# Kernel optimization log

Hardware: AMD Instinct MI355X
Metric: run time of the kernel (lower is better)

## Reference

```python
import jax, jax.numpy as jnp
import numpy as np

L = 2        # n_layers
IN = 172     # in_channels
HID = 128    # hidden_channels
NH = 4       # heads
HD = HID // NH  # per-head dim = 32
TD = 100     # time_dim
V = 400000   # global node table size
N = 150000   # sampled subgraph nodes
E = 500000   # edges per layer
B = 15000    # seed batch size


def setup_inputs() -> dict:
    key = jax.random.key(0)
    ks = jax.random.split(key, 24)
    p = lambda k, shp, s=0.05: jax.random.normal(k, shp, jnp.float32) * s
    inp = {
        "x_all": jax.random.normal(ks[0], (V, IN), jnp.float32),
        "all_node_ids": jax.random.randint(ks[1], (N,), 0, V),
        "edge_src": jax.random.randint(ks[2], (L, E), 0, N),
        "edge_dst": jax.random.randint(ks[3], (L, E), 0, N),
        "dts": jax.random.uniform(ks[4], (L, E), jnp.float32, 0.0, 1e4),
        "batch_size": B,
        # TimeEncode params
        "basis_freq": jnp.asarray(1.0 / 10 ** np.linspace(0, 9, TD), jnp.float32),
        "phase": jnp.zeros((TD,), jnp.float32),
        # input projection
        "Wp": p(ks[5], (IN, HID)), "bp": jnp.zeros((HID,), jnp.float32),
        # per-layer TransformerConv params (stacked over L)
        "Wq": p(ks[6], (L, HID, HID)), "bq": jnp.zeros((L, HID), jnp.float32),
        "Wk": p(ks[7], (L, HID, HID)), "bk": jnp.zeros((L, HID), jnp.float32),
        "Wv": p(ks[8], (L, HID, HID)), "bv": jnp.zeros((L, HID), jnp.float32),
        "We": p(ks[9], (L, TD, HID)),  # lin_edge, bias=False in PyG
        "Wskip": p(ks[10], (L, HID, HID)), "bskip": jnp.zeros((L, HID), jnp.float32),
        "bn_g": jnp.ones((L, HID), jnp.float32), "bn_b": jnp.zeros((L, HID), jnp.float32),
        # classifier head
        "W1": p(ks[11], (HID, HID)), "b1": jnp.zeros((HID,), jnp.float32),
        "g1": jnp.ones((HID,), jnp.float32), "be1": jnp.zeros((HID,), jnp.float32),
        "W2": p(ks[12], (HID, HID // 2)), "b2": jnp.zeros((HID // 2,), jnp.float32),
        "g2": jnp.ones((HID // 2,), jnp.float32), "be2": jnp.zeros((HID // 2,), jnp.float32),
        "W3": p(ks[13], (HID // 2, 1)), "b3": jnp.zeros((1,), jnp.float32),
    }
    return inp


def _bn(x, g, b):
    # BatchNorm1d, training-mode batch statistics (biased variance), eps=1e-5
    m = x.mean(0)
    v = x.var(0)
    return g * (x - m) * jax.lax.rsqrt(v + 1e-5) + b


def reference(x_all, all_node_ids, edge_src, edge_dst, dts, batch_size,
              basis_freq, phase, Wp, bp, Wq, bq, Wk, bk, Wv, bv, We,
              Wskip, bskip, bn_g, bn_b, W1, b1, g1, be1, W2, b2, g2, be2, W3, b3):
    n = all_node_ids.shape[0]
    x = x_all[all_node_ids]                      # [N, IN] gather from global table
    h = jax.nn.relu(x @ Wp + bp)                 # [N, HID]
    inv_sqrt_d = 1.0 / np.sqrt(HD)
    for i in range(L):
        src, dst, dt = edge_src[i], edge_dst[i], dts[i]
        # learnable sinusoidal time encoding of edge delta-t  [E, TD]
        te = jnp.cos(dt[:, None] * basis_freq[None, :] + phase[None, :])
        q = (h @ Wq[i] + bq[i]).reshape(n, NH, HD)
        k = (h @ Wk[i] + bk[i]).reshape(n, NH, HD)
        v = (h @ Wv[i] + bv[i]).reshape(n, NH, HD)
        e = (te @ We[i]).reshape(-1, NH, HD)     # [E, NH, HD]
        kj = k[src] + e                          # key + edge proj (PyG TransformerConv)
        vj = v[src] + e                          # value + edge proj
        alpha = jnp.einsum('ehd,ehd->eh', q[dst], kj) * inv_sqrt_d  # [E, NH]
        # scatter-softmax over edges grouped by destination node
        m = jax.ops.segment_max(alpha, dst, num_segments=n)
        a = jnp.exp(alpha - m[dst])
        s = jax.ops.segment_sum(a, dst, num_segments=n) + 1e-16
        w = a / s[dst]                           # [E, NH]
        agg = jax.ops.segment_sum(w[:, :, None] * vj, dst, num_segments=n)
        out = agg.reshape(n, HID) + h @ Wskip[i] + bskip[i]  # concat heads + root skip
        h = _bn(jax.nn.relu(out), bn_g[i], bn_b[i])          # dropout = identity (eval)
    hb = h[:batch_size]
    z = jax.nn.relu(_bn(hb @ W1 + b1, g1, be1))
    z = jax.nn.relu(_bn(z @ W2 + b2, g2, be2))
    return (z @ W3 + b3)[:, 0]                   # [batch_size]
```

## Files before the change

kernel.cpp:

```cpp
#include <hip/hip_runtime.h>
#include <hip/hip_bf16.h>
#include <math.h>

#define IN_DIM 172
#define HID 128
#define TDIM 100
#define KPAD 192

typedef __attribute__((ext_vector_type(8))) short bf16x8;
typedef __attribute__((ext_vector_type(4))) float f32x4;

static __device__ __forceinline__ ushort f2b(float x) {
  unsigned u = __float_as_uint(x);
  u += 0x7FFFu + ((u >> 16) & 1u);
  return (ushort)(u >> 16);
}
static __device__ __forceinline__ float blo(unsigned w) { return __uint_as_float(w << 16); }
static __device__ __forceinline__ float bhi(unsigned w) { return __uint_as_float(w & 0xffff0000u); }
static __device__ __forceinline__ float b2f(ushort v) { return __uint_as_float((unsigned)v << 16); }

__global__ void k_prep(const float* __restrict__ Wp,
                       const float* __restrict__ Wq, const float* __restrict__ Wk,
                       const float* __restrict__ Wv, const float* __restrict__ Ws,
                       const float* __restrict__ bq, const float* __restrict__ bk,
                       const float* __restrict__ bv, const float* __restrict__ bs,
                       const float* __restrict__ We, const float* __restrict__ W1,
                       ushort* __restrict__ wpt,
                       ushort* __restrict__ wallT0, ushort* __restrict__ wallT1,
                       float* __restrict__ ball0, float* __restrict__ ball1,
                       ushort* __restrict__ wet0, ushort* __restrict__ wet1,
                       ushort* __restrict__ w1t) {
  int i = blockIdx.x * 256 + threadIdx.x;
  if (i < 128 * KPAD) {
    int c = i / KPAD, k = i - c * KPAD;
    wpt[i] = (k < IN_DIM) ? f2b(Wp[k * HID + c]) : (ushort)0;
    return;
  }
  i -= 128 * KPAD;
  if (i < 2 * 512 * 128) {
    int layer = i >> 16;
    int j = i & 65535;
    int col = j >> 7, k = j & 127;
    int m = col >> 7, c = col & 127;
    const float* W = (m == 0) ? Wq : (m == 1) ? Wk : (m == 2) ? Wv : Ws;
    W += (size_t)layer * HID * HID;
    (layer ? wallT1 : wallT0)[j] = f2b(W[k * HID + c]);
    if (k == 0) {
      const float* bb = (m == 0) ? bq : (m == 1) ? bk : (m == 2) ? bv : bs;
      (layer ? ball1 : ball0)[col] = bb[layer * HID + c];
    }
    return;
  }
  i -= 2 * 512 * 128;
  if (i < 2 * 128 * 128) {
    int layer = i >> 14;
    int j = i & 16383;
    int c = j >> 7, t = j & 127;
    (layer ? wet1 : wet0)[j] =
        (t < TDIM) ? f2b(We[((size_t)layer * TDIM + t) * HID + c]) : (ushort)0;
    return;
  }
  i -= 2 * 128 * 128;
  if (i < 128 * 128) {
    int c = i >> 7, k = i & 127;
    w1t[i] = f2b(W1[k * HID + c]);
  }
}

__global__ __launch_bounds__(256) void k_in_mfma(
    const float* __restrict__ x_all, const int* __restrict__ ids,
    const ushort* __restrict__ wpt, const float* __restrict__ bp,
    ushort* __restrict__ h, int n) {
  __shared__ __align__(16) ushort xs[64][200];
  int tid = threadIdx.x;
  long r0 = (long)blockIdx.x * 64;
  for (int i = tid; i < 64 * 28; i += 256) {
    int r = i / 28, c = IN_DIM + (i - r * 28);
    xs[r][c] = 0;
  }
  for (int i = tid; i < 64 * 43; i += 256) {
    int r = i / 43, seg = i - r * 43;
    long row = r0 + r;
    float4 v = make_float4(0.f, 0.f, 0.f, 0.f);
    if (row < n) v = *(const float4*)(x_all + (size_t)ids[row] * IN_DIM + seg * 4);
    ushort4 u;
    u.x = f2b(v.x); u.y = f2b(v.y); u.z = f2b(v.z); u.w = f2b(v.w);
    *(ushort4*)&xs[r][seg * 4] = u;
  }
  __syncthreads();
  int wv = tid >> 6, l = tid & 63;
  int arow = wv * 16 + (l & 15);
  int kb0 = (l >> 4) * 8;
  bf16x8 a[6];
  #pragma unroll
  for (int kk = 0; kk < 6; ++kk) a[kk] = *(const bf16x8*)&xs[arow][kk * 32 + kb0];
  #pragma unroll
  for (int nt = 0; nt < 8; ++nt) {
    int col = nt * 16 + (l & 15);
    const ushort* wcol = wpt + (size_t)col * KPAD + kb0;
    f32x4 acc = {0.f, 0.f, 0.f, 0.f};
    #pragma unroll
    for (int kk = 0; kk < 6; ++kk) {
      bf16x8 bfr = *(const bf16x8*)(wcol + kk * 32);
      acc = __builtin_amdgcn_mfma_f32_16x16x32_bf16(a[kk], bfr, acc, 0, 0, 0);
    }
    float bias = bp[col];
    #pragma unroll
    for (int j = 0; j < 4; ++j) {
      long row = r0 + wv * 16 + (l >> 4) * 4 + j;
      if (row < n) {
        float y = acc[j] + bias;
        h[row * HID + col] = f2b(y > 0.f ? y : 0.f);
      }
    }
  }
}

template <bool BN_IN>
__global__ __launch_bounds__(512) void k_qkvs(
    const ushort* __restrict__ hbf, const ushort* __restrict__ xf,
    const float* __restrict__ sums, const float* __restrict__ bng,
    const float* __restrict__ bnb, float inv_n,
    const ushort* __restrict__ wallT, const float* __restrict__ ball,
    ushort* __restrict__ qb, ushort* __restrict__ kvb,
    ushort* __restrict__ ob, int n) {
  __shared__ __align__(16) ushort hs[128][136];
  __shared__ float As[128], Bs[128];
  int tid = threadIdx.x;
  if (BN_IN) {
    if (tid < 128) {
      float mean = sums[tid] * inv_n;
      float var = sums[128 + tid] * inv_n - mean * mean;
      float A = bng[tid] * rsqrtf(var + 1e-5f);
      As[tid] = A;
      Bs[tid] = bnb[tid] - mean * A;
    }
    __syncthreads();
  }
  long r0 = (long)blockIdx.x * 128;
  for (int i = tid; i < 128 * 16; i += 512) {
    int r = i >> 4, cseg = i & 15;
    long row = r0 + r;
    int c0 = cseg * 8;
    if (BN_IN) {
      ushort4 ua = {0, 0, 0, 0}, ub = {0, 0, 0, 0};
      if (row < n) {
        uint4 xw = *(const uint4*)(xf + row * HID + c0);
        float x0 = blo(xw.x), x1 = bhi(xw.x), x2 = blo(xw.y), x3 = bhi(xw.y);
        float x4 = blo(xw.z), x5 = bhi(xw.z), x6 = blo(xw.w), x7 = bhi(xw.w);
        ua.x = f2b(As[c0 + 0] * fmaxf(x0, 0.f) + Bs[c0 + 0]);
        ua.y = f2b(As[c0 + 1] * fmaxf(x1, 0.f) + Bs[c0 + 1]);
        ua.z = f2b(As[c0 + 2] * fmaxf(x2, 0.f) + Bs[c0 + 2]);
        ua.w = f2b(As[c0 + 3] * fmaxf(x3, 0.f) + Bs[c0 + 3]);
        ub.x = f2b(As[c0 + 4] * fmaxf(x4, 0.f) + Bs[c0 + 4]);
        ub.y = f2b(As[c0 + 5] * fmaxf(x5, 0.f) + Bs[c0 + 5]);
        ub.z = f2b(As[c0 + 6] * fmaxf(x6, 0.f) + Bs[c0 + 6]);
        ub.w = f2b(As[c0 + 7] * fmaxf(x7, 0.f) + Bs[c0 + 7]);
      }
      *(ushort4*)&hs[r][c0] = ua;
      *(ushort4*)&hs[r][c0 + 4] = ub;
    } else {
      bf16x8 zv = {0, 0, 0, 0, 0, 0, 0, 0};
      bf16x8 v = (row < n) ? *(const bf16x8*)&hbf[row * HID + c0] : zv;
      *(bf16x8*)&hs[r][c0] = v;
    }
  }
  int wv = tid >> 6, l = tid & 63;
  int kb0 = (l >> 4) * 8;
  int Cw = wv * 64;
  int m = wv >> 1;
  bf16x8 b[4][4];
  float bias4[4];
  #pragma unroll
  for (int ct = 0; ct < 4; ++ct) {
    int col = Cw + ct * 16 + (l & 15);
    bias4[ct] = ball[col];
    #pragma unroll
    for (int kk = 0; kk < 4; ++kk)
      b[ct][kk] = *(const bf16x8*)&wallT[(size_t)col * 128 + kk * 32 + kb0];
  }
  __syncthreads();
  #pragma unroll 2
  for (int rt = 0; rt < 8; ++rt) {
    bf16x8 a[4];
    #pragma unroll
    for (int kk = 0; kk < 4; ++kk)
      a[kk] = *(const bf16x8*)&hs[rt * 16 + (l & 15)][kk * 32 + kb0];
    f32x4 acc[4];
    #pragma unroll
    for (int ct = 0; ct < 4; ++ct) acc[ct] = (f32x4){0.f, 0.f, 0.f, 0.f};
    #pragma unroll
    for (int kk = 0; kk < 4; ++kk) {
      #pragma unroll
      for (int ct = 0; ct < 4; ++ct)
        acc[ct] = __builtin_amdgcn_mfma_f32_16x16x32_bf16(a[kk], b[ct][kk], acc[ct], 0, 0, 0);
    }
    #pragma unroll
    for (int ct = 0; ct < 4; ++ct) {
      int cc = (wv & 1) * 64 + ct * 16 + (l & 15);
      #pragma unroll
      for (int j = 0; j < 4; ++j) {
        long row = r0 + rt * 16 + (l >> 4) * 4 + j;
        if (row < n) {
          float y = acc[ct][j] + bias4[ct];
          if (m == 0) qb[row * HID + cc] = f2b(y);
          else if (m == 1) kvb[row * 256 + cc] = f2b(y);
          else if (m == 2) kvb[row * 256 + 128 + cc] = f2b(y);
          else ob[row * HID + cc] = f2b(y);
        }
      }
    }
  }
}

__global__ __launch_bounds__(256) void k_mfma128_bn(
    const ushort* __restrict__ xf, const float* __restrict__ sums,
    const float* __restrict__ bng, const float* __restrict__ bnb, float inv_n,
    const ushort* __restrict__ WT, const float* __restrict__ bias,
    float* __restrict__ Y, float* __restrict__ zsums, int n) {
  __shared__ __align__(16) ushort hs[64][136];
  __shared__ float As[128], Bs[128];
  __shared__ float zs1[128], zs2[128];
  int tid = threadIdx.x;
  if (tid < 128) {
    float mean = sums[tid] * inv_n;
    float var = sums[128 + tid] * inv_n - mean * mean;
    float A = bng[tid] * rsqrtf(var + 1e-5f);
    As[tid] = A;
    Bs[tid] = bnb[tid] - mean * A;
    zs1[tid] = 0.f;
    zs2[tid] = 0.f;
  }
  __syncthreads();
  long r0 = (long)blockIdx.x * 64;
  for (int i = tid; i < 64 * 16; i += 256) {
    int r = i >> 4, cseg = i & 15;
    long row = r0 + r;
    int c0 = cseg * 8;
    ushort4 ua = {0, 0, 0, 0}, ub = {0, 0, 0, 0};
    if (row < n) {
      uint4 xw = *(const uint4*)(xf + row * HID + c0);
      float x0 = blo(xw.x), x1 = bhi(xw.x), x2 = blo(xw.y), x3 = bhi(xw.y);
      float x4 = blo(xw.z), x5 = bhi(xw.z), x6 = blo(xw.w), x7 = bhi(xw.w);
      ua.x = f2b(As[c0 + 0] * fmaxf(x0, 0.f) + Bs[c0 + 0]);
      ua.y = f2b(As[c0 + 1] * fmaxf(x1, 0.f) + Bs[c0 + 1]);
      ua.z = f2b(As[c0 + 2] * fmaxf(x2, 0.f) + Bs[c0 + 2]);
      ua.w = f2b(As[c0 + 3] * fmaxf(x3, 0.f) + Bs[c0 + 3]);
      ub.x = f2b(As[c0 + 4] * fmaxf(x4, 0.f) + Bs[c0 + 4]);
      ub.y = f2b(As[c0 + 5] * fmaxf(x5, 0.f) + Bs[c0 + 5]);
      ub.z = f2b(As[c0 + 6] * fmaxf(x6, 0.f) + Bs[c0 + 6]);
      ub.w = f2b(As[c0 + 7] * fmaxf(x7, 0.f) + Bs[c0 + 7]);
    }
    *(ushort4*)&hs[r][c0] = ua;
    *(ushort4*)&hs[r][c0 + 4] = ub;
  }
  __syncthreads();
  int wv = tid >> 6, l = tid & 63;
  int arow = wv * 16 + (l & 15);
  int kb0 = (l >> 4) * 8;
  bf16x8 a[4];
  #pragma unroll
  for (int kk = 0; kk < 4; ++kk) a[kk] = *(const bf16x8*)&hs[arow][kk * 32 + kb0];
  #pragma unroll
  for (int nt = 0; nt < 8; ++nt) {
    int col = nt * 16 + (l & 15);
    const ushort* wcol = WT + (size_t)col * 128 + kb0;
    f32x4 acc = {0.f, 0.f, 0.f, 0.f};
    #pragma unroll
    for (int kk = 0; kk < 4; ++kk) {
      bf16x8 bfr = *(const bf16x8*)(wcol + kk * 32);
      acc = __builtin_amdgcn_mfma_f32_16x16x32_bf16(a[kk], bfr, acc, 0, 0, 0);
    }
    float bs = bias[col];
    float ts = 0.f, tss = 0.f;
    #pragma unroll
    for (int j = 0; j < 4; ++j) {
      long row = r0 + wv * 16 + (l >> 4) * 4 + j;
      if (row < n) {
        float y = acc[j] + bs;
        Y[row * HID + col] = y;
        ts += y;
        tss += y * y;
      }
    }
    atomicAdd(&zs1[col], ts);
    atomicAdd(&zs2[col], tss);
  }
  __syncthreads();
  if (tid < 128) {
    atomicAdd(&zsums[tid], zs1[tid]);
    atomicAdd(&zsums[128 + tid], zs2[tid]);
  }
}

__global__ void k_hist2(const int* __restrict__ dst_all, int* __restrict__ counts,
                        int n, int nE2, int nE) {
  int e = blockIdx.x * 256 + threadIdx.x;
  if (e >= nE2) return;
  int layer = (e >= nE) ? 1 : 0;
  atomicAdd(&counts[layer * n + dst_all[e]], 1);
}

__global__ void k_scan_chunk(const int* __restrict__ counts, int* __restrict__ offs,
                             int* __restrict__ chunkSums, int m) {
  __shared__ int ls[256];
  int t = threadIdx.x;
  int base = blockIdx.x * 1024 + t * 4;
  int v[4];
  #pragma unroll
  for (int j = 0; j < 4; ++j) v[j] = (base + j < m) ? counts[base + j] : 0;
  ls[t] = v[0] + v[1] + v[2] + v[3];
  __syncthreads();
  for (int off = 1; off < 256; off <<= 1) {
    int x = (t >= off) ? ls[t - off] : 0;
    __syncthreads();
    ls[t] += x;
    __syncthreads();
  }
  int run = (t == 0) ? 0 : ls[t - 1];
  if (t == 255) chunkSums[blockIdx.x] = ls[255];
  #pragma unroll
  for (int j = 0; j < 4; ++j) {
    if (base + j < m) offs[base + j] = run;
    run += v[j];
  }
}

__global__ __launch_bounds__(512) void k_scan_tops(int* __restrict__ chunkSums, int nchunks) {
  __shared__ int ls[512];
  int t = threadIdx.x;
  ls[t] = (t < nchunks) ? chunkSums[t] : 0;
  __syncthreads();
  for (int off = 1; off < 512; off <<= 1) {
    int x = (t >= off) ? ls[t - off] : 0;
    __syncthreads();
    ls[t] += x;
    __syncthreads();
  }
  int excl = (t == 0) ? 0 : ls[t - 1];
  if (t < nchunks) chunkSums[t] = excl;
}

__global__ void k_scan_add(int* __restrict__ offs, const int* __restrict__ chunkSums,
                           int m, int totalE) {
  int i = blockIdx.x * 256 + threadIdx.x;
  if (i < m) offs[i] += chunkSums[i >> 10];
  if (i == 0) offs[m] = totalE;
}

__global__ void k_scatter2(const int* __restrict__ src_all, const int* __restrict__ dst_all,
                           const float* __restrict__ dts_all, const int* __restrict__ offs,
                           int* __restrict__ cursor, uint2* __restrict__ edata,
                           int n, int nE2, int nE) {
  int e = blockIdx.x * 256 + threadIdx.x;
  if (e >= nE2) return;
  int layer = (e >= nE) ? 1 : 0;
  int d = layer * n + dst_all[e];
  int pos = offs[d] + atomicAdd(&cursor[d], 1);
  edata[pos] = make_uint2((unsigned)src_all[e], __float_as_uint(dts_all[e]));
}

__global__ __launch_bounds__(256) void k_te_mfma(
    const uint2* __restrict__ edata, const float* __restrict__ freq,
    const float* __restrict__ phase, const ushort* __restrict__ wet,
    ushort* __restrict__ eb, int nE) {
  __shared__ __align__(16) ushort te[64][136];
  __shared__ float dt_s[64];
  __shared__ float fr_s[128], ph_s[128];
  int tid = threadIdx.x;
  if (tid < 128) {
    fr_s[tid] = (tid < TDIM) ? freq[tid] : 0.f;
    ph_s[tid] = (tid < TDIM) ? phase[tid] : 0.f;
  }
  long e0 = (long)blockIdx.x << 6;
  if (tid < 64) dt_s[tid] = (e0 + tid < nE) ? __uint_as_float(edata[e0 + tid].y) : 0.f;
  __syncthreads();
  for (int i = tid; i < 64 * 128; i += 256) {
    int el = i >> 7, t = i & 127;
    float val = (t < TDIM) ? __cosf(dt_s[el] * fr_s[t] + ph_s[t]) : 0.f;
    te[el][t] = f2b(val);
  }
  __syncthreads();
  int wv = tid >> 6, l = tid & 63;
  int arow = wv * 16 + (l & 15);
  int kb0 = (l >> 4) * 8;
  bf16x8 a[4];
  #pragma unroll
  for (int kk = 0; kk < 4; ++kk) a[kk] = *(const bf16x8*)&te[arow][kk * 32 + kb0];
  __syncthreads();
  #pragma unroll
  for (int nt = 0; nt < 8; ++nt) {
    int col = nt * 16 + (l & 15);
    const ushort* wcol = wet + (size_t)col * 128 + kb0;
    f32x4 acc = {0.f, 0.f, 0.f, 0.f};
    #pragma unroll
    for (int kk = 0; kk < 4; ++kk) {
      bf16x8 bfr = *(const bf16x8*)(wcol + kk * 32);
      acc = __builtin_amdgcn_mfma_f32_16x16x32_bf16(a[kk], bfr, acc, 0, 0, 0);
    }
    #pragma unroll
    for (int j = 0; j < 4; ++j)
      te[wv * 16 + (l >> 4) * 4 + j][col] = f2b(acc[j]);
  }
  __syncthreads();
  for (int i = tid; i < 64 * 16; i += 256) {
    int r = i >> 4, cs = i & 15;
    long row = e0 + r;
    if (row < nE) *(bf16x8*)&eb[row * 128 + cs * 8] = *(const bf16x8*)&te[r][cs * 8];
  }
}

__global__ void k_attn(const int* __restrict__ offs_l, const uint2* __restrict__ edata,
                       int bias, const ushort* __restrict__ eb,
                       const ushort* __restrict__ qb, const ushort* __restrict__ kvb,
                       ushort* __restrict__ ob, int n) {
  int d = (blockIdx.x * 256 + threadIdx.x) >> 4;
  if (d >= n) return;
  int cl = threadIdx.x & 15;
  int c0 = cl * 8;
  int beg = offs_l[d], end = offs_l[d + 1];
  if (beg == end) return;
  const ushort* ebl = eb - (size_t)bias * HID;
  uint4 qw = *(const uint4*)(qb + (size_t)d * HID + c0);
  float q0 = blo(qw.x), q1 = bhi(qw.x), q2 = blo(qw.y), q3 = bhi(qw.y);
  float q4 = blo(qw.z), q5 = bhi(qw.z), q6 = blo(qw.w), q7 = bhi(qw.w);
  float s = 0.f;
  float a0 = 0.f, a1 = 0.f, a2 = 0.f, a3 = 0.f, a4 = 0.f, a5 = 0.f, a6 = 0.f, a7 = 0.f;
  int pos = beg;
  for (; pos + 2 <= end; pos += 2) {
    int svA = (int)edata[pos].x;
    int svB = (int)edata[pos + 1].x;
    uint4 kwA = *(const uint4*)(kvb + (size_t)svA * 256 + c0);
    uint4 vwA = *(const uint4*)(kvb + (size_t)svA * 256 + 128 + c0);
    uint4 ewA = *(const uint4*)(ebl + (size_t)pos * HID + c0);
    uint4 kwB = *(const uint4*)(kvb + (size_t)svB * 256 + c0);
    uint4 vwB = *(const uint4*)(kvb + (size_t)svB * 256 + 128 + c0);
    uint4 ewB = *(const uint4*)(ebl + (size_t)(pos + 1) * HID + c0);
    float eA0 = blo(ewA.x), eA1 = bhi(ewA.x), eA2 = blo(ewA.y), eA3 = bhi(ewA.y);
    float eA4 = blo(ewA.z), eA5 = bhi(ewA.z), eA6 = blo(ewA.w), eA7 = bhi(ewA.w);
    float eB0 = blo(ewB.x), eB1 = bhi(ewB.x), eB2 = blo(ewB.y), eB3 = bhi(ewB.y);
    float eB4 = blo(ewB.z), eB5 = bhi(ewB.z), eB6 = blo(ewB.w), eB7 = bhi(ewB.w);
    float pA = q0 * (blo(kwA.x) + eA0) + q1 * (bhi(kwA.x) + eA1) +
               q2 * (blo(kwA.y) + eA2) + q3 * (bhi(kwA.y) + eA3) +
               q4 * (blo(kwA.z) + eA4) + q5 * (bhi(kwA.z) + eA5) +
               q6 * (blo(kwA.w) + eA6) + q7 * (bhi(kwA.w) + eA7);
    float pB = q0 * (blo(kwB.x) + eB0) + q1 * (bhi(kwB.x) + eB1) +
               q2 * (blo(kwB.y) + eB2) + q3 * (bhi(kwB.y) + eB3) +
               q4 * (blo(kwB.z) + eB4) + q5 * (bhi(kwB.z) + eB5) +
               q6 * (blo(kwB.w) + eB6) + q7 * (bhi(kwB.w) + eB7);
    pA += __shfl_xor(pA, 1);
    pA += __shfl_xor(pA, 2);
    pB += __shfl_xor(pB, 1);
    pB += __shfl_xor(pB, 2);
    float peA = __expf(pA * 0.17677669529663687f);
    float peB = __expf(pB * 0.17677669529663687f);
    s += peA + peB;
    a0 += peA * (blo(vwA.x) + eA0) + peB * (blo(vwB.x) + eB0);
    a1 += peA * (bhi(vwA.x) + eA1) + peB * (bhi(vwB.x) + eB1);
    a2 += peA * (blo(vwA.y) + eA2) + peB * (blo(vwB.y) + eB2);
    a3 += peA * (bhi(vwA.y) + eA3) + peB * (bhi(vwB.y) + eB3);
    a4 += peA * (blo(vwA.z) + eA4) + peB * (blo(vwB.z) + eB4);
    a5 += peA * (bhi(vwA.z) + eA5) + peB * (bhi(vwB.z) + eB5);
    a6 += peA * (blo(vwA.w) + eA6) + peB * (blo(vwB.w) + eB6);
    a7 += peA * (bhi(vwA.w) + eA7) + peB * (bhi(vwB.w) + eB7);
  }
  if (pos < end) {
    int sv = (int)edata[pos].x;
    uint4 kw = *(const uint4*)(kvb + (size_t)sv * 256 + c0);
    uint4 vw = *(const uint4*)(kvb + (size_t)sv * 256 + 128 + c0);
    uint4 ew = *(const uint4*)(ebl + (size_t)pos * HID + c0);
    float e0 = blo(ew.x), e1 = bhi(ew.x), e2 = blo(ew.y), e3 = bhi(ew.y);
    float e4 = blo(ew.z), e5 = bhi(ew.z), e6 = blo(ew.w), e7 = bhi(ew.w);
    float p = q0 * (blo(kw.x) + e0) + q1 * (bhi(kw.x) + e1) +
              q2 * (blo(kw.y) + e2) + q3 * (bhi(kw.y) + e3) +
              q4 * (blo(kw.z) + e4) + q5 * (bhi(kw.z) + e5) +
              q6 * (blo(kw.w) + e6) + q7 * (bhi(kw.w) + e7);
    p += __shfl_xor(p, 1);
    p += __shfl_xor(p, 2);
    float pe = __expf(p * 0.17677669529663687f);
    s += pe;
    a0 += pe * (blo(vw.x) + e0);
    a1 += pe * (bhi(vw.x) + e1);
    a2 += pe * (blo(vw.y) + e2);
    a3 += pe * (bhi(vw.y) + e3);
    a4 += pe * (blo(vw.z) + e4);
    a5 += pe * (bhi(vw.z) + e5);
    a6 += pe * (blo(vw.w) + e6);
    a7 += pe * (bhi(vw.w) + e7);
  }
  float inv = 1.f / (s + 1e-16f);
  uint4* o = (uint4*)(ob + (size_t)d * HID + c0);
  uint4 ow = *o;
  float y0 = blo(ow.x) + a0 * inv, y1 = bhi(ow.x) + a1 * inv;
  float y2 = blo(ow.y) + a2 * inv, y3 = bhi(ow.y) + a3 * inv;
  float y4 = blo(ow.z) + a4 * inv, y5 = bhi(ow.z) + a5 * inv;
  float y6 = blo(ow.w) + a6 * inv, y7 = bhi(ow.w) + a7 * inv;
  uint4 w;
  w.x = (unsigned)f2b(y0) | ((unsigned)f2b(y1) << 16);
  w.y = (unsigned)f2b(y2) | ((unsigned)f2b(y3) << 16);
  w.z = (unsigned)f2b(y4) | ((unsigned)f2b(y5) << 16);
  w.w = (unsigned)f2b(y6) | ((unsigned)f2b(y7) << 16);
  *o = w;
}

__global__ void k_bn_reduce_b(const ushort* __restrict__ X, int n,
                              float* __restrict__ sums) {
  int col = threadIdx.x & 127;
  int rloc = threadIdx.x >> 7;
  float s = 0.f, s2 = 0.f;
  for (long r = (long)blockIdx.x * 2 + rloc; r < n; r += (long)gridDim.x * 2) {
    float v = b2f(X[r * HID + col]);
    v = v > 0.f ? v : 0.f;
    s += v; s2 += v * v;
  }
  __shared__ float ls[256], ls2[256];
  ls[threadIdx.x] = s; ls2[threadIdx.x] = s2;
  __syncthreads();
  if (rloc == 0) {
    s += ls[128 + col]; s2 += ls2[128 + col];
    atomicAdd(&sums[col], s);
    atomicAdd(&sums[128 + col], s2);
  }
}

__global__ __launch_bounds__(256) void k_gemm_64(
    const float* __restrict__ X, const float* __restrict__ sums,
    const float* __restrict__ g, const float* __restrict__ be, float inv_n,
    const float* __restrict__ W, const float* __restrict__ b,
    float* __restrict__ Y, float* __restrict__ zsums, int n) {
  __shared__ float xs[16][HID];
  __shared__ float As[128], Bs[128];
  __shared__ float zs1[64], zs2[64];
  if (threadIdx.x < 128) {
    int c = threadIdx.x;
    float mean = sums[c] * inv_n;
    float var = sums[128 + c] * inv_n - mean * mean;
    float A = g[c] * rsqrtf(var + 1e-5f);
    As[c] = A;
    Bs[c] = be[c] - mean * A;
    if (c < 64) { zs1[c] = 0.f; zs2[c] = 0.f; }
  }
  __syncthreads();
  int r0 = blockIdx.x * 16;
  for (int idx = threadIdx.x; idx < 16 * HID; idx += 256) {
    int r = idx >> 7, c = idx & 127;
    int row = r0 + r;
    float v = (row < n) ? X[(size_t)row * HID + c] : 0.f;
    v = As[c] * v + Bs[c];
    xs[r][c] = v > 0.f ? v : 0.f;
  }
  __syncthreads();
  int col = threadIdx.x & 63;
  int rg = threadIdx.x >> 6;
  float acc[4] = {0.f, 0.f, 0.f, 0.f};
  #pragma unroll 4
  for (int kk = 0; kk < HID; ++kk) {
    float w = W[kk * 64 + col];
    #pragma unroll
    for (int j = 0; j < 4; ++j) acc[j] += xs[rg + 4 * j][kk] * w;
  }
  float bias = b[col];
  float ts = 0.f, tss = 0.f;
  #pragma unroll
  for (int j = 0; j < 4; ++j) {
    int row = r0 + rg + 4 * j;
    if (row < n) {
      float y = acc[j] + bias;
      Y[(size_t)row * 64 + col] = y;
      ts += y;
      tss += y * y;
    }
  }
  atomicAdd(&zs1[col], ts);
  atomicAdd(&zs2[col], tss);
  __syncthreads();
  if (threadIdx.x < 64) {
    atomicAdd(&zsums[threadIdx.x], zs1[threadIdx.x]);
    atomicAdd(&zsums[64 + threadIdx.x], zs2[threadIdx.x]);
  }
}

__global__ __launch_bounds__(256) void k_final(
    const float* __restrict__ z2, const float* __restrict__ sums,
    const float* __restrict__ g2, const float* __restrict__ be2, float inv_n,
    const float* __restrict__ W3, const float* __restrict__ b3,
    float* __restrict__ out, int n) {
  int wave = threadIdx.x >> 6, lane = threadIdx.x & 63;
  int row = blockIdx.x * 4 + wave;
  if (row >= n) return;
  float z = z2[(size_t)row * 64 + lane];
  float mean = sums[lane] * inv_n;
  float var = sums[64 + lane] * inv_n - mean * mean;
  float v = g2[lane] * (z - mean) * rsqrtf(var + 1e-5f) + be2[lane];
  v = v > 0.f ? v : 0.f;
  float pv = v * W3[lane];
  pv += __shfl_xor(pv, 1);
  pv += __shfl_xor(pv, 2);
  pv += __shfl_xor(pv, 4);
  pv += __shfl_xor(pv, 8);
  pv += __shfl_xor(pv, 16);
  pv += __shfl_xor(pv, 32);
  if (lane == 0) out[row] = pv + b3[0];
}

extern "C" void kernel_launch(void* const* d_in, const int* in_sizes, int n_in,
                              void* d_out, int out_size, void* d_ws, size_t ws_size,
                              hipStream_t stream) {
  const float* x_all = (const float*)d_in[0];
  const int* ids = (const int*)d_in[1];
  const int* esrc = (const int*)d_in[2];
  const int* edst = (const int*)d_in[3];
  const float* dts = (const float*)d_in[4];
  const float* freq = (const float*)d_in[6];
  const float* phase = (const float*)d_in[7];
  const float* Wp = (const float*)d_in[8];
  const float* bp = (const float*)d_in[9];
  const float* Wq = (const float*)d_in[10];
  const float* bq = (const float*)d_in[11];
  const float* Wk = (const float*)d_in[12];
  const float* bk = (const float*)d_in[13];
  const float* Wv = (const float*)d_in[14];
  const float* bv = (const float*)d_in[15];
  const float* We = (const float*)d_in[16];
  const float* Wskip = (const float*)d_in[17];
  const float* bskip = (const float*)d_in[18];
  const float* bn_g = (const float*)d_in[19];
  const float* bn_b = (const float*)d_in[20];
  const float* W1 = (const float*)d_in[21];
  const float* b1 = (const float*)d_in[22];
  const float* g1 = (const float*)d_in[23];
  const float* be1 = (const float*)d_in[24];
  const float* W2 = (const float*)d_in[25];
  const float* b2 = (const float*)d_in[26];
  const float* g2 = (const float*)d_in[27];
  const float* be2 = (const float*)d_in[28];
  const float* W3 = (const float*)d_in[29];
  const float* b3 = (const float*)d_in[30];

  size_t n = (size_t)in_sizes[1];
  size_t nE = (size_t)in_sizes[2] / 2;
  size_t nE2 = nE * 2;
  int B = out_size;

  char* pc = (char*)d_ws;
  auto alloc = [&](size_t bytes) { char* r = pc; pc += (bytes + 255) & ~(size_t)255; return r; };
  ushort* h    = (ushort*)alloc(n * HID * 2);
  ushort* qb   = (ushort*)alloc(n * HID * 2);
  ushort* kvb  = (ushort*)alloc(n * 256 * 2);
  ushort* ob0  = (ushort*)alloc(n * HID * 2);
  ushort* ob1  = (ushort*)alloc(n * HID * 2);
  ushort* eb0  = (ushort*)alloc(nE * HID * 2);
  ushort* eb1  = (ushort*)alloc(nE * HID * 2);
  uint2* edata = (uint2*)alloc(nE2 * 8);
  int* offs    = (int*)alloc((2 * n + 2) * 4);
  int* chunkS  = (int*)alloc(512 * 4);
  size_t zbytes = 4 * n * 4 + 4 * 256 * 4;
  char* zb = alloc(zbytes);
  int* counts = (int*)zb;
  int* cursor = counts + 2 * n;
  float* sumsL0 = (float*)(cursor + 2 * n);
  float* sumsL1 = sumsL0 + 256;
  float* sumsZ1 = sumsL1 + 256;
  float* sumsZ2 = sumsZ1 + 256;
  ushort* wpt    = (ushort*)alloc(128 * KPAD * 2);
  ushort* wallT0 = (ushort*)alloc(512 * 128 * 2);
  ushort* wallT1 = (ushort*)alloc(512 * 128 * 2);
  float* ball0   = (float*)alloc(512 * 4);
  float* ball1   = (float*)alloc(512 * 4);
  ushort* wet0   = (ushort*)alloc(128 * 128 * 2);
  ushort* wet1   = (ushort*)alloc(128 * 128 * 2);
  ushort* w1t    = (ushort*)alloc(128 * 128 * 2);
  float* z1      = (float*)alloc((size_t)B * HID * 4);
  float* z2      = (float*)alloc((size_t)B * 64 * 4);

  int gn64 = (int)((n + 63) / 64);
  int gn128 = (int)((n + 127) / 128);
  int ge2 = (int)((nE2 + 255) / 256);
  int eblk = (int)((nE + 63) / 64);
  int m2 = (int)(2 * n);
  int nchunks = (m2 + 1023) / 1024;
  float inv_nf = 1.f / (float)n;
  float inv_bf = 1.f / (float)B;

  hipMemsetAsync(zb, 0, zbytes, stream);
  k_prep<<<(128 * KPAD + 2 * 512 * 128 + 2 * 128 * 128 + 128 * 128 + 255) / 256, 256, 0, stream>>>(
      Wp, Wq, Wk, Wv, Wskip, bq, bk, bv, bskip, We, W1,
      wpt, wallT0, wallT1, ball0, ball1, wet0, wet1, w1t);

  k_hist2<<<ge2, 256, 0, stream>>>(edst, counts, (int)n, (int)nE2, (int)nE);
  k_scan_chunk<<<nchunks, 256, 0, stream>>>(counts, offs, chunkS, m2);
  k_scan_tops<<<1, 512, 0, stream>>>(chunkS, nchunks);
  k_scan_add<<<(m2 + 255) / 256, 256, 0, stream>>>(offs, chunkS, m2, (int)nE2);
  k_scatter2<<<ge2, 256, 0, stream>>>(esrc, edst, dts, offs, cursor, edata,
                                      (int)n, (int)nE2, (int)nE);

  k_te_mfma<<<eblk, 256, 0, stream>>>(edata, freq, phase, wet0, eb0, (int)nE);

  k_in_mfma<<<gn64, 256, 0, stream>>>(x_all, ids, wpt, bp, h, (int)n);

  for (int i = 0; i < 2; ++i) {
    const ushort* wallT = i ? wallT1 : wallT0;
    const float* ball = i ? ball1 : ball0;
    const ushort* eb = i ? eb1 : eb0;
    ushort* ob = i ? ob1 : ob0;
    int bias = i * (int)nE;

    if (i == 1)
      k_te_mfma<<<eblk, 256, 0, stream>>>(edata + nE, freq, phase, wet1, eb1, (int)nE);

    if (i == 0)
      k_qkvs<false><<<gn128, 512, 0, stream>>>(h, nullptr, nullptr, nullptr, nullptr, 0.f,
                                               wallT, ball, qb, kvb, ob, (int)n);
    else
      k_qkvs<true><<<gn128, 512, 0, stream>>>(nullptr, ob0, sumsL0, bn_g, bn_b, inv_nf,
                                              wallT, ball, qb, kvb, ob, (int)n);

    k_attn<<<(int)((n + 15) / 16), 256, 0, stream>>>(offs + (size_t)i * n, edata, bias,
                                                     eb, qb, kvb, ob, (int)n);
    k_bn_reduce_b<<<512, 256, 0, stream>>>(ob, (int)n, i ? sumsL1 : sumsL0);
  }

  k_mfma128_bn<<<(B + 63) / 64, 256, 0, stream>>>(ob1, sumsL1, bn_g + HID, bn_b + HID,
                                                  inv_nf, w1t, b1, z1, sumsZ1, B);
  k_gemm_64<<<(B + 15) / 16, 256, 0, stream>>>(z1, sumsZ1, g1, be1, inv_bf, W2, b2,
                                               z2, sumsZ2, B);
  k_final<<<(B + 3) / 4, 256, 0, stream>>>(z2, sumsZ2, g2, be2, inv_bf, W3, b3,
                                           (float*)d_out, B);
}
```

Baseline: 971.2 us.

## Sort destination nodes by in-degree to balance attention kernel work

Adds a degree histogram, a scan and a scatter that build a per-layer permutation grouping destination nodes by in-degree (capped at 63). The attention kernel then processes nodes in that order, so the 16-lane groups sharing a wavefront have similar edge counts. This aims to cut divergence and idle lanes caused by Poisson-distributed degrees. The cost is three extra small kernels, atomics, and an indirect perm lookup that scatters the output writes and q loads.

```diff
diff --git a/kernel.cpp b/kernel.cpp
--- a/kernel.cpp
+++ b/kernel.cpp
@@ -360,6 +360,43 @@
   edata[pos] = make_uint2((unsigned)src_all[e], __float_as_uint(dts_all[e]));
 }
 
+__global__ void k_deghist(const int* __restrict__ counts, int* __restrict__ dhist,
+                          int n2, int n) {
+  int d = blockIdx.x * 256 + threadIdx.x;
+  if (d >= n2) return;
+  int bin = counts[d];
+  if (bin > 63) bin = 63;
+  atomicAdd(&dhist[(d >= n ? 64 : 0) + bin], 1);
+}
+
+__global__ __launch_bounds__(128) void k_degscan(int* __restrict__ dhist, int n) {
+  __shared__ int ls[128];
+  int t = threadIdx.x;
+  ls[t] = dhist[t];
+  __syncthreads();
+  for (int off = 1; off < 64; off <<= 1) {
+    int x = ((t & 63) >= off) ? ls[t - off] : 0;
+    __syncthreads();
+    ls[t] += x;
+    __syncthreads();
+  }
+  int excl = ((t & 63) == 0) ? 0 : ls[t - 1];
+  dhist[t] = excl + ((t >= 64) ? n : 0);
+}
+
+__global__ void k_degscatter(const int* __restrict__ counts, const int* __restrict__ dhist,
+                             int* __restrict__ dcur, int* __restrict__ perm,
+                             int n2, int n) {
+  int d = blockIdx.x * 256 + threadIdx.x;
+  if (d >= n2) return;
+  int layer = (d >= n) ? 1 : 0;
+  int bin = counts[d];
+  if (bin > 63) bin = 63;
+  int idx = layer * 64 + bin;
+  int pos = dhist[idx] + atomicAdd(&dcur[idx], 1);
+  perm[pos] = layer ? d - n : d;
+}
+
 __global__ __launch_bounds__(256) void k_te_mfma(
     const uint2* __restrict__ edata, const float* __restrict__ freq,
     const float* __restrict__ phase, const ushort* __restrict__ wet,
@@ -410,12 +447,13 @@
   }
 }
 
-__global__ void k_attn(const int* __restrict__ offs_l, const uint2* __restrict__ edata,
-                       int bias, const ushort* __restrict__ eb,
-                       const ushort* __restrict__ qb, const ushort* __restrict__ kvb,
-                       ushort* __restrict__ ob, int n) {
-  int d = (blockIdx.x * 256 + threadIdx.x) >> 4;
-  if (d >= n) return;
+__global__ void k_attn(const int* __restrict__ perm, const int* __restrict__ offs_l,
+                       const uint2* __restrict__ edata, int bias,
+                       const ushort* __restrict__ eb, const ushort* __restrict__ qb,
+                       const ushort* __restrict__ kvb, ushort* __restrict__ ob, int n) {
+  int idx = (blockIdx.x * 256 + threadIdx.x) >> 4;
+  if (idx >= n) return;
+  int d = perm[idx];
   int cl = threadIdx.x & 15;
   int c0 = cl * 8;
   int beg = offs_l[d], end = offs_l[d + 1];
@@ -654,7 +692,8 @@
   uint2* edata = (uint2*)alloc(nE2 * 8);
   int* offs    = (int*)alloc((2 * n + 2) * 4);
   int* chunkS  = (int*)alloc(512 * 4);
-  size_t zbytes = 4 * n * 4 + 4 * 256 * 4;
+  int* perm    = (int*)alloc(2 * n * 4);
+  size_t zbytes = 4 * n * 4 + 4 * 256 * 4 + 256 * 4;
   char* zb = alloc(zbytes);
   int* counts = (int*)zb;
   int* cursor = counts + 2 * n;
@@ -662,6 +701,8 @@
   float* sumsL1 = sumsL0 + 256;
   float* sumsZ1 = sumsL1 + 256;
   float* sumsZ2 = sumsZ1 + 256;
+  int* dhist = (int*)(sumsZ2 + 256);
+  int* dcur  = dhist + 128;
   ushort* wpt    = (ushort*)alloc(128 * KPAD * 2);
   ushort* wallT0 = (ushort*)alloc(512 * 128 * 2);
   ushort* wallT1 = (ushort*)alloc(512 * 128 * 2);
@@ -678,6 +719,7 @@
   int ge2 = (int)((nE2 + 255) / 256);
   int eblk = (int)((nE + 63) / 64);
   int m2 = (int)(2 * n);
+  int gn2 = (m2 + 255) / 256;
   int nchunks = (m2 + 1023) / 1024;
   float inv_nf = 1.f / (float)n;
   float inv_bf = 1.f / (float)B;
@@ -694,6 +736,10 @@
   k_scatter2<<<ge2, 256, 0, stream>>>(esrc, edst, dts, offs, cursor, edata,
                                       (int)n, (int)nE2, (int)nE);
 
+  k_deghist<<<gn2, 256, 0, stream>>>(counts, dhist, m2, (int)n);
+  k_degscan<<<1, 128, 0, stream>>>(dhist, (int)n);
+  k_degscatter<<<gn2, 256, 0, stream>>>(counts, dhist, dcur, perm, m2, (int)n);
+
   k_te_mfma<<<eblk, 256, 0, stream>>>(edata, freq, phase, wet0, eb0, (int)nE);
 
   k_in_mfma<<<gn64, 256, 0, stream>>>(x_all, ids, wpt, bp, h, (int)n);
@@ -715,7 +761,8 @@
       k_qkvs<true><<<gn128, 512, 0, stream>>>(nullptr, ob0, sumsL0, bn_g, bn_b, inv_nf,
                                               wallT, ball, qb, kvb, ob, (int)n);
 
-    k_attn<<<(int)((n + 15) / 16), 256, 0, stream>>>(offs + (size_t)i * n, edata, bias,
+    k_attn<<<(int)((n + 15) / 16), 256, 0, stream>>>(perm + (size_t)i * n,
+                                                     offs + (size_t)i * n, edata, bias,
                                                      eb, qb, kvb, ob, (int)n);
     k_bn_reduce_b<<<512, 256, 0, stream>>>(ob, (int)n, i ? sumsL1 : sumsL0);
   }
```

After: 2.865 ms. 195% more time.
